# Kernel optimization log

Measured on AMD Instinct MI355X. Metric: run time of the kernel, lower is better.

## Reference

```python
import jax, jax.numpy as jnp
import numpy as np

N = 50000      # nodes
E = 625000     # directed edges
F_IN, H1, H2, OUT = 128, 128, 64, 50


def setup_inputs() -> dict:
    key = jax.random.key(0)
    ks = jax.random.split(key, 5)
    x = jax.random.normal(ks[0], (N, F_IN), dtype=jnp.float32)
    edge_index = jax.random.randint(ks[1], (2, E), 0, N, dtype=jnp.int64)
    W1 = jax.random.normal(ks[2], (F_IN, H1), dtype=jnp.float32) * 0.05
    b1 = jnp.zeros((H1,), jnp.float32)
    W2 = jax.random.normal(ks[3], (H1, H2), dtype=jnp.float32) * 0.05
    b2 = jnp.zeros((H2,), jnp.float32)
    Wh = jax.random.normal(ks[4], (H2, OUT), dtype=jnp.float32) * 0.05
    bh = jnp.zeros((OUT,), jnp.float32)
    return {"x": x, "edge_index": edge_index, "W1": W1, "b1": b1,
            "W2": W2, "b2": b2, "Wh": Wh, "bh": bh}


def _gcn_conv(h, W, b, src, dst, dinv, n):
    # h' = D^{-1/2} A_hat D^{-1/2} (h W) + b, A_hat includes self-loops
    h = h @ W                                   # [n, out]
    coef = (dinv[src] * dinv[dst])[:, None]      # [e, 1]
    agg = jax.ops.segment_sum(h[src] * coef, dst, num_segments=n)
    return agg + b


def reference(x, edge_index, W1, b1, W2, b2, Wh, bh):
    n = x.shape[0]
    loops = jnp.arange(n, dtype=edge_index.dtype)
    src = jnp.concatenate([edge_index[0], loops])
    dst = jnp.concatenate([edge_index[1], loops])
    # symmetric GCN normalization: deg over destinations (incl. self-loops)
    deg = jax.ops.segment_sum(jnp.ones(src.shape[0], x.dtype), dst, num_segments=n)
    dinv = jnp.where(deg > 0, jax.lax.rsqrt(deg), 0.0)
    # dropout is a no-op in eval mode (training=False)
    h = _gcn_conv(x, W1, b1, src, dst, dinv, n)
    h = jax.nn.relu(h)
    h = _gcn_conv(h, W2, b2, src, dst, dinv, n)
    h = jax.nn.relu(h)
    return h @ Wh + bh
```

## Files before the change

kernel.cpp:

```cpp
#include <hip/hip_runtime.h>

#define F_IN 128
#define HH1 128
#define HH2 64
#define FOUT 50
#define EB 256
#define NBUCK_MAX 256

typedef __attribute__((ext_vector_type(8))) short short8;
typedef __attribute__((ext_vector_type(4))) short s16x4;
typedef __attribute__((ext_vector_type(4))) float f32x4;

__device__ inline short f2bf(float f) {
    union { float f; unsigned u; } v; v.f = f;
    unsigned r = v.u + 0x7fffu + ((v.u >> 16) & 1u);
    return (short)(r >> 16);
}
__device__ inline float bf2f(short s) {
    union { float f; unsigned u; } v; v.u = ((unsigned)(unsigned short)s) << 16;
    return v.f;
}

__device__ inline int detect64(const unsigned* raw) {
    __shared__ int s_is64;
    if (threadIdx.x == 0) s_is64 = 1;
    __syncthreads();
    if (raw[2 * threadIdx.x + 1] != 0u) atomicAnd(&s_is64, 0);
    __syncthreads();
    return s_is64;
}

__global__ __launch_bounds__(256) void bucket_count(
    const int* __restrict__ raw, int E, int nbuck, int* __restrict__ parthist,
    const float* __restrict__ W1, const float* __restrict__ W2,
    const float* __restrict__ Wh, short* __restrict__ W1t,
    short* __restrict__ W2t, short* __restrict__ Wht) {
    __shared__ int hist[NBUCK_MAX];
    const int tid = threadIdx.x;
    int is64 = detect64((const unsigned*)raw);
    for (int k = tid; k < nbuck; k += 256) hist[k] = 0;
    __syncthreads();
    const int CH = (E + EB - 1) / EB;
    const int e0 = blockIdx.x * CH, e1 = min(E, e0 + CH);
    for (int e = e0 + tid; e < e1; e += 256) {
        int d = is64 ? raw[2 * (long)E + 2 * e] : raw[E + e];
        atomicAdd(&hist[d >> 8], 1);
    }
    __syncthreads();
    for (int k = tid; k < nbuck; k += 256) parthist[blockIdx.x * nbuck + k] = hist[k];
    const int T1 = HH1 * F_IN, T2 = HH2 * HH1, T3 = 64 * HH2;
    int idx = blockIdx.x * 256 + tid;
    if (idx < T1) {
        int c = idx / F_IN, k = idx - c * F_IN;
        W1t[idx] = f2bf(W1[(long)k * HH1 + c]);
    } else if (idx < T1 + T2) {
        int i = idx - T1;
        int c = i / HH1, k = i - c * HH1;
        W2t[i] = f2bf(W2[(long)k * HH2 + c]);
    } else if (idx < T1 + T2 + T3) {
        int i = idx - T1 - T2;
        int c = i / HH2, k = i - c * HH2;
        Wht[i] = f2bf((c < FOUT) ? Wh[(long)k * FOUT + c] : 0.f);
    }
}

__global__ __launch_bounds__(256) void bucket_scan(
    int* __restrict__ parthist, int* __restrict__ bbase, int nbuck, int E) {
    __shared__ int sh[256];
    const int k = threadIdx.x;
    int sum = 0;
    if (k < nbuck)
        for (int b = 0; b < EB; ++b) sum += parthist[b * nbuck + k];
    int v = (k < nbuck) ? sum : 0;
    sh[k] = v;
    __syncthreads();
    for (int off = 1; off < 256; off <<= 1) {
        int t = (k >= off) ? sh[k - off] : 0;
        __syncthreads();
        sh[k] += t;
        __syncthreads();
    }
    int base = sh[k] - v;
    if (k < nbuck) bbase[k] = base;
    if (k == 0) bbase[nbuck] = E;
    if (k < nbuck) {
        int run = base;
        for (int b = 0; b < EB; ++b) {
            int t = parthist[b * nbuck + k];
            parthist[b * nbuck + k] = run;
            run += t;
        }
    }
}

__global__ __launch_bounds__(256) void bucket_scatter(
    const int* __restrict__ raw, int E, int nbuck,
    const int* __restrict__ parthist, int2* __restrict__ tmp) {
    __shared__ int cur[NBUCK_MAX];
    const int tid = threadIdx.x;
    int is64 = detect64((const unsigned*)raw);
    for (int k = tid; k < nbuck; k += 256) cur[k] = parthist[blockIdx.x * nbuck + k];
    __syncthreads();
    const int CH = (E + EB - 1) / EB;
    const int e0 = blockIdx.x * CH, e1 = min(E, e0 + CH);
    for (int e = e0 + tid; e < e1; e += 256) {
        int s, d;
        if (is64) {
            s = raw[2 * e];
            d = raw[2 * (long)E + 2 * e];
        } else {
            s = raw[e];
            d = raw[E + e];
        }
        int pos = atomicAdd(&cur[d >> 8], 1);
        tmp[pos] = make_int2(s, d);
    }
}

__global__ __launch_bounds__(256) void bucket_finalize(
    const int2* __restrict__ tmp, const int* __restrict__ bbase,
    int* __restrict__ rowptr, float* __restrict__ dinv,
    int* __restrict__ csr_src, int n, int nbuck) {
    __shared__ int deg[256];
    __shared__ int cur[256];
    __shared__ int sh[256];
    const int k = blockIdx.x;
    const int tid = threadIdx.x;
    const int b0 = bbase[k], b1 = bbase[k + 1];
    deg[tid] = 0;
    __syncthreads();
    for (int e = b0 + tid; e < b1; e += 256) atomicAdd(&deg[tmp[e].y & 255], 1);
    __syncthreads();
    int v = deg[tid];
    sh[tid] = v;
    __syncthreads();
    for (int off = 1; off < 256; off <<= 1) {
        int t = (tid >= off) ? sh[tid - off] : 0;
        __syncthreads();
        sh[tid] += t;
        __syncthreads();
    }
    int excl = sh[tid] - v;
    cur[tid] = excl;
    int node = (k << 8) + tid;
    if (node < n) {
        rowptr[node] = b0 + excl;
        dinv[node] = rsqrtf((float)v + 1.0f);
    }
    if (k == 0 && tid == 0) rowptr[n] = bbase[nbuck];
    __syncthreads();
    for (int e = b0 + tid; e < b1; e += 256) {
        int2 sd = tmp[e];
        int p = atomicAdd(&cur[sd.y & 255], 1);
        csr_src[b0 + p] = sd.x;
    }
}

template <int K, int NC, bool IN_BF16, bool OUT_F32, bool BIAS>
__global__ __launch_bounds__(256) void mfma_gemm(const void* __restrict__ Xv,
                                                 const short* __restrict__ Wt,
                                                 const float* __restrict__ bias,
                                                 void* __restrict__ Yv, int M, int NCOUT) {
    const int tid = threadIdx.x;
    const int wave = tid >> 6;
    const int lane = tid & 63;
    const int l15 = lane & 15;
    const int kg = lane >> 4;
    const int rowbase = blockIdx.x * 64 + wave * 16;
    const int arow = rowbase + l15;
    constexpr int KS = K / 32;

    short8 af[KS];
    if (arow < M) {
        if (IN_BF16) {
            const short* xr = (const short*)Xv + (long)arow * K + kg * 8;
#pragma unroll
            for (int ks = 0; ks < KS; ++ks) af[ks] = *(const short8*)(xr + ks * 32);
        } else {
            const float* xr = (const float*)Xv + (long)arow * K + kg * 8;
#pragma unroll
            for (int ks = 0; ks < KS; ++ks) {
                float4 f0 = *(const float4*)(xr + ks * 32);
                float4 f1 = *(const float4*)(xr + ks * 32 + 4);
                short8 a;
                a[0] = f2bf(f0.x); a[1] = f2bf(f0.y); a[2] = f2bf(f0.z); a[3] = f2bf(f0.w);
                a[4] = f2bf(f1.x); a[5] = f2bf(f1.y); a[6] = f2bf(f1.z); a[7] = f2bf(f1.w);
                af[ks] = a;
            }
        }
    } else {
#pragma unroll
        for (int ks = 0; ks < KS; ++ks) af[ks] = (short8)0;
    }

    const int crowb = rowbase + kg * 4;
#pragma unroll
    for (int ct = 0; ct < NC / 16; ++ct) {
        const int col = ct * 16 + l15;
        const short* wr = Wt + (long)col * K + kg * 8;
        f32x4 acc = {0.f, 0.f, 0.f, 0.f};
#pragma unroll
        for (int ks = 0; ks < KS; ++ks) {
            short8 bf = *(const short8*)(wr + ks * 32);
            acc = __builtin_amdgcn_mfma_f32_16x16x32_bf16(af[ks], bf, acc, 0, 0, 0);
        }
        if (OUT_F32) {
            float* Y = (float*)Yv;
            float bv = BIAS ? bias[col] : 0.f;
#pragma unroll
            for (int j = 0; j < 4; ++j) {
                int r = crowb + j;
                if (r < M && col < NCOUT) Y[(long)r * NCOUT + col] = acc[j] + bv;
            }
        } else {
            short* Y = (short*)Yv;
#pragma unroll
            for (int j = 0; j < 4; ++j) {
                int r = crowb + j;
                if (r < M) Y[(long)r * NC + col] = f2bf(acc[j]);
            }
        }
    }
}

template <int LPN, int NPB>
__global__ __launch_bounds__(256) void agg_csr_bf16(const short* __restrict__ h,
                                                    const int* __restrict__ rowptr,
                                                    const int* __restrict__ csr_src,
                                                    const float* __restrict__ dinv,
                                                    const float* __restrict__ bias,
                                                    short* __restrict__ agg, int n) {
    const int tid = threadIdx.x;
    const int node = blockIdx.x * NPB + tid / LPN;
    const int lane = tid % LPN;
    if (node >= n) return;
    const s16x4* __restrict__ h4 = (const s16x4*)h;

    const float di = dinv[node];
    float4 acc = ((const float4*)bias)[lane];
    float cs = di * di;
    s16x4 hv = h4[(long)node * LPN + lane];
    acc.x = fmaf(cs, bf2f(hv[0]), acc.x);
    acc.y = fmaf(cs, bf2f(hv[1]), acc.y);
    acc.z = fmaf(cs, bf2f(hv[2]), acc.z);
    acc.w = fmaf(cs, bf2f(hv[3]), acc.w);

    int e = rowptr[node];
    const int end = rowptr[node + 1];
    for (; e + 3 < end; e += 4) {
        int s0 = csr_src[e];
        int s1 = csr_src[e + 1];
        int s2 = csr_src[e + 2];
        int s3 = csr_src[e + 3];
        s16x4 v0 = h4[(long)s0 * LPN + lane];
        s16x4 v1 = h4[(long)s1 * LPN + lane];
        s16x4 v2 = h4[(long)s2 * LPN + lane];
        s16x4 v3 = h4[(long)s3 * LPN + lane];
        float c0 = dinv[s0] * di;
        float c1 = dinv[s1] * di;
        float c2 = dinv[s2] * di;
        float c3 = dinv[s3] * di;
        acc.x = fmaf(c0, bf2f(v0[0]), acc.x);
        acc.y = fmaf(c0, bf2f(v0[1]), acc.y);
        acc.z = fmaf(c0, bf2f(v0[2]), acc.z);
        acc.w = fmaf(c0, bf2f(v0[3]), acc.w);
        acc.x = fmaf(c1, bf2f(v1[0]), acc.x);
        acc.y = fmaf(c1, bf2f(v1[1]), acc.y);
        acc.z = fmaf(c1, bf2f(v1[2]), acc.z);
        acc.w = fmaf(c1, bf2f(v1[3]), acc.w);
        acc.x = fmaf(c2, bf2f(v2[0]), acc.x);
        acc.y = fmaf(c2, bf2f(v2[1]), acc.y);
        acc.z = fmaf(c2, bf2f(v2[2]), acc.z);
        acc.w = fmaf(c2, bf2f(v2[3]), acc.w);
        acc.x = fmaf(c3, bf2f(v3[0]), acc.x);
        acc.y = fmaf(c3, bf2f(v3[1]), acc.y);
        acc.z = fmaf(c3, bf2f(v3[2]), acc.z);
        acc.w = fmaf(c3, bf2f(v3[3]), acc.w);
    }
    for (; e < end; ++e) {
        int s0 = csr_src[e];
        float c0 = dinv[s0] * di;
        s16x4 v0 = h4[(long)s0 * LPN + lane];
        acc.x = fmaf(c0, bf2f(v0[0]), acc.x);
        acc.y = fmaf(c0, bf2f(v0[1]), acc.y);
        acc.z = fmaf(c0, bf2f(v0[2]), acc.z);
        acc.w = fmaf(c0, bf2f(v0[3]), acc.w);
    }
    s16x4 o;
    o[0] = f2bf(fmaxf(acc.x, 0.f));
    o[1] = f2bf(fmaxf(acc.y, 0.f));
    o[2] = f2bf(fmaxf(acc.z, 0.f));
    o[3] = f2bf(fmaxf(acc.w, 0.f));
    ((s16x4*)agg)[(long)node * LPN + lane] = o;
}

static inline size_t al256(size_t x) { return (x + 255) & ~(size_t)255; }

extern "C" void kernel_launch(void* const* d_in, const int* in_sizes, int n_in,
                              void* d_out, int out_size, void* d_ws, size_t ws_size,
                              hipStream_t stream) {
    const float* x    = (const float*)d_in[0];
    const int*   eraw = (const int*)d_in[1];
    const float* W1   = (const float*)d_in[2];
    const float* b1   = (const float*)d_in[3];
    const float* W2   = (const float*)d_in[4];
    const float* b2   = (const float*)d_in[5];
    const float* Wh   = (const float*)d_in[6];
    const float* bh   = (const float*)d_in[7];
    float* out = (float*)d_out;
    const int n = in_sizes[0] / F_IN;
    const int E = in_sizes[1] / 2;
    const int nbuck = (n + 255) >> 8;

    char* p = (char*)d_ws;
    float* dinv     = (float*)p; p += al256((size_t)n * 4);
    int*   rowptr   = (int*)p;   p += al256((size_t)(n + 1) * 4);
    int*   parthist = (int*)p;   p += al256((size_t)EB * nbuck * 4);
    int*   bbase    = (int*)p;   p += al256((size_t)(nbuck + 1) * 4);
    int*   csr_src  = (int*)p;   p += al256((size_t)E * 4);
    short* W1t      = (short*)p; p += al256((size_t)HH1 * F_IN * 2);
    short* W2t      = (short*)p; p += al256((size_t)HH2 * HH1 * 2);
    short* Whtp     = (short*)p; p += al256((size_t)64 * HH2 * 2);
    short* bigA     = (short*)p; p += al256((size_t)n * HH1 * 2);
    short* bigB     = (short*)p;
    int2* tmp   = (int2*)bigA;
    short* h1   = bigA;
    short* agg1 = bigB;
    short* h2   = bigA;
    short* agg2 = bigA + (size_t)n * HH2;

    dim3 blk(256);
    bucket_count<<<EB, blk, 0, stream>>>(eraw, E, nbuck, parthist, W1, W2, Wh, W1t, W2t, Whtp);
    bucket_scan<<<1, blk, 0, stream>>>(parthist, bbase, nbuck, E);
    bucket_scatter<<<EB, blk, 0, stream>>>(eraw, E, nbuck, parthist, tmp);
    bucket_finalize<<<nbuck, blk, 0, stream>>>(tmp, bbase, rowptr, dinv, csr_src, n, nbuck);

    const int gblocks = (n + 63) / 64;
    mfma_gemm<F_IN, HH1, false, false, false><<<gblocks, blk, 0, stream>>>(x, W1t, nullptr, h1, n, HH1);
    agg_csr_bf16<32, 8><<<(n + 7) / 8, blk, 0, stream>>>(h1, rowptr, csr_src, dinv, b1, agg1, n);
    mfma_gemm<HH1, HH2, true, false, false><<<gblocks, blk, 0, stream>>>(agg1, W2t, nullptr, h2, n, HH2);
    agg_csr_bf16<16, 16><<<(n + 15) / 16, blk, 0, stream>>>(h2, rowptr, csr_src, dinv, b2, agg2, n);
    mfma_gemm<HH2, 64, true, true, true><<<gblocks, blk, 0, stream>>>(agg2, Whtp, bh, out, n, FOUT);
}
```

Measured before the change: 148.8 us.

## Fuse CSR aggregation with following GEMM via shared-memory tile and MFMA

Replaces the separate aggregation kernels and the second and third GEMM launches with a fused agg_mm kernel. Each block aggregates 16 nodes into a shared-memory bf16 tile, then multiplies that tile by the next weight matrix with MFMA and writes h2 or the final output directly. This removes two kernel launches and the global round trip of the aggregated intermediate. In exchange, lanes per node change (16 lanes with 8 features each for layer 1), the edge loop unroll drops from 4 to 2, and each block reloads the weights from global memory.

```diff
diff --git a/kernel.cpp b/kernel.cpp
--- a/kernel.cpp
+++ b/kernel.cpp
@@ -223,75 +223,124 @@
     }
 }
 
-template <int LPN, int NPB>
-__global__ __launch_bounds__(256) void agg_csr_bf16(const short* __restrict__ h,
-                                                    const int* __restrict__ rowptr,
-                                                    const int* __restrict__ csr_src,
-                                                    const float* __restrict__ dinv,
-                                                    const float* __restrict__ bias,
-                                                    short* __restrict__ agg, int n) {
-    const int tid = threadIdx.x;
-    const int node = blockIdx.x * NPB + tid / LPN;
-    const int lane = tid % LPN;
-    if (node >= n) return;
-    const s16x4* __restrict__ h4 = (const s16x4*)h;
-
-    const float di = dinv[node];
-    float4 acc = ((const float4*)bias)[lane];
-    float cs = di * di;
-    s16x4 hv = h4[(long)node * LPN + lane];
-    acc.x = fmaf(cs, bf2f(hv[0]), acc.x);
-    acc.y = fmaf(cs, bf2f(hv[1]), acc.y);
-    acc.z = fmaf(cs, bf2f(hv[2]), acc.z);
-    acc.w = fmaf(cs, bf2f(hv[3]), acc.w);
-
-    int e = rowptr[node];
-    const int end = rowptr[node + 1];
-    for (; e + 3 < end; e += 4) {
-        int s0 = csr_src[e];
-        int s1 = csr_src[e + 1];
-        int s2 = csr_src[e + 2];
-        int s3 = csr_src[e + 3];
-        s16x4 v0 = h4[(long)s0 * LPN + lane];
-        s16x4 v1 = h4[(long)s1 * LPN + lane];
-        s16x4 v2 = h4[(long)s2 * LPN + lane];
-        s16x4 v3 = h4[(long)s3 * LPN + lane];
-        float c0 = dinv[s0] * di;
-        float c1 = dinv[s1] * di;
-        float c2 = dinv[s2] * di;
-        float c3 = dinv[s3] * di;
-        acc.x = fmaf(c0, bf2f(v0[0]), acc.x);
-        acc.y = fmaf(c0, bf2f(v0[1]), acc.y);
-        acc.z = fmaf(c0, bf2f(v0[2]), acc.z);
-        acc.w = fmaf(c0, bf2f(v0[3]), acc.w);
-        acc.x = fmaf(c1, bf2f(v1[0]), acc.x);
-        acc.y = fmaf(c1, bf2f(v1[1]), acc.y);
-        acc.z = fmaf(c1, bf2f(v1[2]), acc.z);
-        acc.w = fmaf(c1, bf2f(v1[3]), acc.w);
-        acc.x = fmaf(c2, bf2f(v2[0]), acc.x);
-        acc.y = fmaf(c2, bf2f(v2[1]), acc.y);
-        acc.z = fmaf(c2, bf2f(v2[2]), acc.z);
-        acc.w = fmaf(c2, bf2f(v2[3]), acc.w);
-        acc.x = fmaf(c3, bf2f(v3[0]), acc.x);
-        acc.y = fmaf(c3, bf2f(v3[1]), acc.y);
-        acc.z = fmaf(c3, bf2f(v3[2]), acc.z);
-        acc.w = fmaf(c3, bf2f(v3[3]), acc.w);
-    }
-    for (; e < end; ++e) {
-        int s0 = csr_src[e];
-        float c0 = dinv[s0] * di;
-        s16x4 v0 = h4[(long)s0 * LPN + lane];
-        acc.x = fmaf(c0, bf2f(v0[0]), acc.x);
-        acc.y = fmaf(c0, bf2f(v0[1]), acc.y);
-        acc.z = fmaf(c0, bf2f(v0[2]), acc.z);
-        acc.w = fmaf(c0, bf2f(v0[3]), acc.w);
-    }
-    s16x4 o;
-    o[0] = f2bf(fmaxf(acc.x, 0.f));
-    o[1] = f2bf(fmaxf(acc.y, 0.f));
-    o[2] = f2bf(fmaxf(acc.z, 0.f));
-    o[3] = f2bf(fmaxf(acc.w, 0.f));
-    ((s16x4*)agg)[(long)node * LPN + lane] = o;
+template <int FPL>
+__device__ inline void gather2(const short* p0, const short* p1, float c0,
+                               float c1, float* acc) {
+    if constexpr (FPL == 8) {
+        short8 v0 = *(const short8*)p0;
+        short8 v1 = *(const short8*)p1;
+#pragma unroll
+        for (int j = 0; j < 8; ++j) acc[j] = fmaf(c0, bf2f(v0[j]), acc[j]);
+#pragma unroll
+        for (int j = 0; j < 8; ++j) acc[j] = fmaf(c1, bf2f(v1[j]), acc[j]);
+    } else {
+        s16x4 v0 = *(const s16x4*)p0;
+        s16x4 v1 = *(const s16x4*)p1;
+#pragma unroll
+        for (int j = 0; j < 4; ++j) acc[j] = fmaf(c0, bf2f(v0[j]), acc[j]);
+#pragma unroll
+        for (int j = 0; j < 4; ++j) acc[j] = fmaf(c1, bf2f(v1[j]), acc[j]);
+    }
+}
+template <int FPL>
+__device__ inline void gather1(const short* p0, float c0, float* acc) {
+    if constexpr (FPL == 8) {
+        short8 v0 = *(const short8*)p0;
+#pragma unroll
+        for (int j = 0; j < 8; ++j) acc[j] = fmaf(c0, bf2f(v0[j]), acc[j]);
+    } else {
+        s16x4 v0 = *(const s16x4*)p0;
+#pragma unroll
+        for (int j = 0; j < 4; ++j) acc[j] = fmaf(c0, bf2f(v0[j]), acc[j]);
+    }
+}
+
+template <int FW, bool OUT_F32>
+__global__ __launch_bounds__(256) void agg_mm(
+    const short* __restrict__ h, const int* __restrict__ rowptr,
+    const int* __restrict__ csr_src, const float* __restrict__ dinv,
+    const float* __restrict__ bias_pre, const short* __restrict__ Wt,
+    const float* __restrict__ bias_post, void* __restrict__ Yv, int n,
+    int ncreal) {
+    constexpr int FPL = FW / 16;
+    constexpr int LDW = FW + 8;
+    constexpr int KS = FW / 32;
+    __shared__ short tile[16][LDW];
+    const int tid = threadIdx.x;
+    const int grp = tid >> 4;
+    const int l16 = tid & 15;
+    const int node = blockIdx.x * 16 + grp;
+
+    float acc[FPL];
+#pragma unroll
+    for (int j = 0; j < FPL; ++j) acc[j] = 0.f;
+
+    if (node < n) {
+        const float di = dinv[node];
+#pragma unroll
+        for (int j = 0; j < FPL; ++j) acc[j] = bias_pre[l16 * FPL + j];
+        gather1<FPL>(h + (long)node * FW + l16 * FPL, di * di, acc);
+        int e = rowptr[node];
+        const int end = rowptr[node + 1];
+        for (; e + 1 < end; e += 2) {
+            int s0 = csr_src[e];
+            int s1 = csr_src[e + 1];
+            float c0 = dinv[s0] * di;
+            float c1 = dinv[s1] * di;
+            gather2<FPL>(h + (long)s0 * FW + l16 * FPL,
+                         h + (long)s1 * FW + l16 * FPL, c0, c1, acc);
+        }
+        if (e < end) {
+            int s0 = csr_src[e];
+            gather1<FPL>(h + (long)s0 * FW + l16 * FPL, dinv[s0] * di, acc);
+        }
+    }
+    if constexpr (FPL == 8) {
+        short8 o;
+#pragma unroll
+        for (int j = 0; j < 8; ++j) o[j] = f2bf(fmaxf(acc[j], 0.f));
+        *(short8*)&tile[grp][l16 * 8] = o;
+    } else {
+        s16x4 o;
+#pragma unroll
+        for (int j = 0; j < 4; ++j) o[j] = f2bf(fmaxf(acc[j], 0.f));
+        *(s16x4*)&tile[grp][l16 * 4] = o;
+    }
+    __syncthreads();
+
+    const int wave = tid >> 6;
+    const int lane = tid & 63;
+    const int l15 = lane & 15;
+    const int kg = lane >> 4;
+    const int col = wave * 16 + l15;
+    short8 af[KS];
+#pragma unroll
+    for (int ks = 0; ks < KS; ++ks)
+        af[ks] = *(const short8*)&tile[l15][kg * 8 + ks * 32];
+    f32x4 c2 = {0.f, 0.f, 0.f, 0.f};
+    const short* wr = Wt + (long)col * FW + kg * 8;
+#pragma unroll
+    for (int ks = 0; ks < KS; ++ks) {
+        short8 bfr = *(const short8*)(wr + ks * 32);
+        c2 = __builtin_amdgcn_mfma_f32_16x16x32_bf16(af[ks], bfr, c2, 0, 0, 0);
+    }
+    const int rb = blockIdx.x * 16 + kg * 4;
+    if (OUT_F32) {
+        float* Y = (float*)Yv;
+#pragma unroll
+        for (int j = 0; j < 4; ++j) {
+            int g = rb + j;
+            if (g < n && col < ncreal)
+                Y[(long)g * ncreal + col] = c2[j] + bias_post[col];
+        }
+    } else {
+        short* Y = (short*)Yv;
+#pragma unroll
+        for (int j = 0; j < 4; ++j) {
+            int g = rb + j;
+            if (g < n) Y[(long)g * 64 + col] = f2bf(c2[j]);
+        }
+    }
 }
 
 static inline size_t al256(size_t x) { return (x + 255) & ~(size_t)255; }
@@ -325,9 +374,7 @@
     short* bigB     = (short*)p;
     int2* tmp   = (int2*)bigA;
     short* h1   = bigA;
-    short* agg1 = bigB;
-    short* h2   = bigA;
-    short* agg2 = bigA + (size_t)n * HH2;
+    short* h2   = bigB;
 
     dim3 blk(256);
     bucket_count<<<EB, blk, 0, stream>>>(eraw, E, nbuck, parthist, W1, W2, Wh, W1t, W2t, Whtp);
@@ -335,10 +382,10 @@
     bucket_scatter<<<EB, blk, 0, stream>>>(eraw, E, nbuck, parthist, tmp);
     bucket_finalize<<<nbuck, blk, 0, stream>>>(tmp, bbase, rowptr, dinv, csr_src, n, nbuck);
 
-    const int gblocks = (n + 63) / 64;
-    mfma_gemm<F_IN, HH1, false, false, false><<<gblocks, blk, 0, stream>>>(x, W1t, nullptr, h1, n, HH1);
-    agg_csr_bf16<32, 8><<<(n + 7) / 8, blk, 0, stream>>>(h1, rowptr, csr_src, dinv, b1, agg1, n);
-    mfma_gemm<HH1, HH2, true, false, false><<<gblocks, blk, 0, stream>>>(agg1, W2t, nullptr, h2, n, HH2);
-    agg_csr_bf16<16, 16><<<(n + 15) / 16, blk, 0, stream>>>(h2, rowptr, csr_src, dinv, b2, agg2, n);
-    mfma_gemm<HH2, 64, true, true, true><<<gblocks, blk, 0, stream>>>(agg2, Whtp, bh, out, n, FOUT);
-}
+    mfma_gemm<F_IN, HH1, false, false, false><<<(n + 63) / 64, blk, 0, stream>>>(
+        x, W1t, nullptr, h1, n, HH1);
+    agg_mm<HH1, false><<<(n + 15) / 16, blk, 0, stream>>>(
+        h1, rowptr, csr_src, dinv, b1, W2t, nullptr, h2, n, HH2);
+    agg_mm<HH2, true><<<(n + 15) / 16, blk, 0, stream>>>(
+        h2, rowptr, csr_src, dinv, b2, Whtp, bh, out, n, FOUT);
+}
```

New measurement: 137.7 us. -7.4%, faster.
